# Optimization experiments

Measured on AMD Instinct MI355X. Metric: run time of the kernel, lower is better.

## Reference

```python
import jax, jax.numpy as jnp
import numpy as np

EPS = 1e-5

def layer_norm(x, g, b):
    mu = jnp.mean(x, axis=-1, keepdims=True)
    var = jnp.mean(jnp.square(x - mu), axis=-1, keepdims=True)
    return (x - mu) * jax.lax.rsqrt(var + EPS) * g + b

def setup_inputs() -> dict:
    B, T, C, H = 8, 1024, 1024, 16
    hs = C // H
    key = jax.random.key(0)
    ks = jax.random.split(key, 12)
    s = 0.02
    return {
        "x": jax.random.normal(ks[0], (B, T, C), dtype=jnp.float32),
        # per-head projections, stacked: [H, C, hs]
        "wq": jax.random.normal(ks[1], (H, C, hs), dtype=jnp.float32) * s,
        "wk": jax.random.normal(ks[2], (H, C, hs), dtype=jnp.float32) * s,
        "wv": jax.random.normal(ks[3], (H, C, hs), dtype=jnp.float32) * s,
        "w_proj": jax.random.normal(ks[4], (C, C), dtype=jnp.float32) * s,
        "b_proj": jnp.zeros((C,), dtype=jnp.float32),
        "ln1_g": jnp.ones((C,), dtype=jnp.float32),
        "ln1_b": jnp.zeros((C,), dtype=jnp.float32),
        "ln2_g": jnp.ones((C,), dtype=jnp.float32),
        "ln2_b": jnp.zeros((C,), dtype=jnp.float32),
        "w1": jax.random.normal(ks[5], (C, 4 * C), dtype=jnp.float32) * s,
        "b1": jnp.zeros((4 * C,), dtype=jnp.float32),
        "w2": jax.random.normal(ks[6], (4 * C, C), dtype=jnp.float32) * s,
        "b2": jnp.zeros((C,), dtype=jnp.float32),
    }

def reference(x, wq, wk, wv, w_proj, b_proj, ln1_g, ln1_b, ln2_g, ln2_b, w1, b1, w2, b2):
    B, T, C = x.shape
    # --- self-attention (pre-norm) ---
    h = layer_norm(x, ln1_g, ln1_b)                      # [B,T,C]
    q = jnp.einsum('btc,hcd->bhtd', h, wq)               # [B,H,T,hs]
    k = jnp.einsum('btc,hcd->bhtd', h, wk)
    v = jnp.einsum('btc,hcd->bhtd', h, wv)
    # NOTE: original scales by C**-0.5 with C = n_embed (not head_size)
    scores = jnp.einsum('bhtd,bhsd->bhts', q, k) * (C ** -0.5)
    causal = jnp.tril(jnp.ones((T, T), dtype=bool))
    scores = jnp.where(causal, scores, -jnp.inf)
    att = jax.nn.softmax(scores, axis=-1)                # dropout is identity (eval)
    out = jnp.einsum('bhts,bhsd->bhtd', att, v)          # [B,H,T,hs]
    out = out.transpose(0, 2, 1, 3).reshape(B, T, C)     # concat heads
    x = x + out @ w_proj + b_proj
    # --- feed-forward (pre-norm) ---
    h2 = layer_norm(x, ln2_g, ln2_b)
    x = x + jax.nn.relu(h2 @ w1 + b1) @ w2 + b2
    return x
```

## Files before the change

### kernel.cpp

```cpp
#include <hip/hip_runtime.h>
#include <cstdint>

typedef __attribute__((ext_vector_type(8))) __bf16 bf16x8;
typedef __attribute__((ext_vector_type(4))) float f32x4;

__device__ __forceinline__ unsigned short f2bf(float f) {
  union { float f; unsigned int u; } v; v.f = f;
  unsigned int u = v.u;
  return (unsigned short)((u + 0x7FFFu + ((u >> 16) & 1u)) >> 16);
}

__device__ __forceinline__ void load_lds16(const unsigned short* g, unsigned short* l) {
  __builtin_amdgcn_global_load_lds(
      (const __attribute__((address_space(1))) unsigned int*)g,
      (__attribute__((address_space(3))) unsigned int*)l, 16, 0, 0);
}

__global__ void transpose_f2b(const float* __restrict__ src, unsigned short* __restrict__ dst,
                              int K, int N, long sStride, long dStride) {
  __shared__ float tile[32][33];
  src += (long)blockIdx.z * sStride;
  dst += (long)blockIdx.z * dStride;
  const int nt = blockIdx.x * 32, kt = blockIdx.y * 32;
  const int tx = threadIdx.x & 31, ty = threadIdx.x >> 5;
#pragma unroll
  for (int i = 0; i < 4; i++)
    tile[ty + 8 * i][tx] = src[(long)(kt + ty + 8 * i) * N + nt + tx];
  __syncthreads();
#pragma unroll
  for (int i = 0; i < 4; i++)
    dst[(long)(nt + ty + 8 * i) * K + kt + tx] = f2bf(tile[tx][ty + 8 * i]);
}

__global__ void transpose_qkv(const float* __restrict__ wq, const float* __restrict__ wk,
                              const float* __restrict__ wv, unsigned short* __restrict__ dst) {
  __shared__ float tile[32][33];
  const int which = blockIdx.z >> 4, slice = blockIdx.z & 15;
  const float* src = (which == 0 ? wq : which == 1 ? wk : wv) + (long)slice * 65536;
  unsigned short* d = dst + (long)which * 1048576 + (long)slice * 65536;
  const int nt = blockIdx.x * 32, kt = blockIdx.y * 32;
  const int tx = threadIdx.x & 31, ty = threadIdx.x >> 5;
#pragma unroll
  for (int i = 0; i < 4; i++)
    tile[ty + 8 * i][tx] = src[(long)(kt + ty + 8 * i) * 64 + nt + tx];
  __syncthreads();
#pragma unroll
  for (int i = 0; i < 4; i++)
    d[(long)(nt + ty + 8 * i) * 1024 + kt + tx] = f2bf(tile[tx][ty + 8 * i]);
}

__global__ __launch_bounds__(256, 4) void ln_kernel(const float* __restrict__ x,
                                                    const float* __restrict__ g,
                                                    const float* __restrict__ b,
                                                    unsigned short* __restrict__ out) {
  const int row = blockIdx.x, tid = threadIdx.x;
  const int wave = tid >> 6, lane = tid & 63;
  const float4 xv = *(const float4*)&x[(long)row * 1024 + tid * 4];
  float s1 = xv.x + xv.y + xv.z + xv.w;
  float s2 = xv.x * xv.x + xv.y * xv.y + xv.z * xv.z + xv.w * xv.w;
#pragma unroll
  for (int m = 1; m < 64; m <<= 1) { s1 += __shfl_xor(s1, m); s2 += __shfl_xor(s2, m); }
  __shared__ float a1[4], a2[4];
  if (lane == 0) { a1[wave] = s1; a2[wave] = s2; }
  __syncthreads();
  s1 = a1[0] + a1[1] + a1[2] + a1[3];
  s2 = a2[0] + a2[1] + a2[2] + a2[3];
  const float mu = s1 * (1.f / 1024.f);
  const float var = s2 * (1.f / 1024.f) - mu * mu;
  const float rs = rsqrtf(var + 1e-5f);
  const float4 gv = *(const float4*)&g[tid * 4];
  const float4 bv = *(const float4*)&b[tid * 4];
  ushort4 o;
  o.x = f2bf((xv.x - mu) * rs * gv.x + bv.x);
  o.y = f2bf((xv.y - mu) * rs * gv.y + bv.y);
  o.z = f2bf((xv.z - mu) * rs * gv.z + bv.z);
  o.w = f2bf((xv.w - mu) * rs * gv.w + bv.w);
  *(ushort4*)&out[(long)row * 1024 + tid * 4] = o;
}

#define EPI_QKV 0
#define EPI_F32 1
#define EPI_RELU 2

template <int EPI>
__global__ __launch_bounds__(256, 2) void gemm_bt(
    const unsigned short* __restrict__ A, const unsigned short* __restrict__ Bt,
    int M, int N, int K,
    const float* __restrict__ bias, const float* __restrict__ resid,
    float* __restrict__ outF, unsigned short* __restrict__ outB,
    unsigned short* __restrict__ qb, unsigned short* __restrict__ kb,
    unsigned short* __restrict__ vTb) {
  __shared__ __attribute__((aligned(16))) unsigned short Alds[128 * 64];
  __shared__ __attribute__((aligned(16))) unsigned short Blds[128 * 64];
  const int tid = threadIdx.x;
  const int wave = tid >> 6, lane = tid & 63;
  const int quad = lane >> 4, l15 = lane & 15;
  const long tM = (long)blockIdx.x * 128;
  const long tN = (long)blockIdx.y * 128;
  const int wm = (wave >> 1) * 64, wn = (wave & 1) * 64;

  const unsigned short* aP[4];
  const unsigned short* bP[4];
  unsigned short* lA[4];
  unsigned short* lB[4];
#pragma unroll
  for (int qq = 0; qq < 4; qq++) {
    int p = (qq * 4 + wave) * 64 + lane;
    int m = p >> 3;
    int kc = (p & 7) ^ (m & 7);
    aP[qq] = A + (tM + m) * K + kc * 8;
    bP[qq] = Bt + (tN + m) * K + kc * 8;
    lA[qq] = Alds + (qq * 4 + wave) * 512;
    lB[qq] = Blds + (qq * 4 + wave) * 512;
  }

  f32x4 acc[4][4];
#pragma unroll
  for (int i = 0; i < 4; i++)
#pragma unroll
    for (int j = 0; j < 4; j++) acc[i][j] = (f32x4){0.f, 0.f, 0.f, 0.f};

  for (int k0 = 0; k0 < K; k0 += 64) {
    __syncthreads();
#pragma unroll
    for (int qq = 0; qq < 4; qq++) {
      load_lds16(aP[qq], lA[qq]);
      load_lds16(bP[qq], lB[qq]);
      aP[qq] += 64;
      bP[qq] += 64;
    }
    __syncthreads();
#pragma unroll
    for (int ks = 0; ks < 2; ks++) {
      bf16x8 af[4], bfr[4];
#pragma unroll
      for (int mt = 0; mt < 4; mt++) {
        int ml = wm + mt * 16 + l15;
        int pc = (ks * 4 + quad) ^ (ml & 7);
        af[mt] = *(const bf16x8*)&Alds[(ml * 8 + pc) * 8];
      }
#pragma unroll
      for (int nt = 0; nt < 4; nt++) {
        int nl = wn + nt * 16 + l15;
        int pc = (ks * 4 + quad) ^ (nl & 7);
        bfr[nt] = *(const bf16x8*)&Blds[(nl * 8 + pc) * 8];
      }
#pragma unroll
      for (int mt = 0; mt < 4; mt++)
#pragma unroll
        for (int nt = 0; nt < 4; nt++)
          acc[mt][nt] = __builtin_amdgcn_mfma_f32_16x16x32_bf16(af[mt], bfr[nt], acc[mt][nt], 0, 0, 0);
    }
  }

#pragma unroll
  for (int mt = 0; mt < 4; mt++) {
#pragma unroll
    for (int nt = 0; nt < 4; nt++) {
      const long col = tN + wn + nt * 16 + l15;
      const long row0 = tM + wm + mt * 16 + quad * 4;
      if (EPI == EPI_F32) {
        const float bv = bias[col];
#pragma unroll
        for (int r = 0; r < 4; r++) {
          long idx = (row0 + r) * N + col;
          outF[idx] = acc[mt][nt][r] + bv + resid[idx];
        }
      } else if (EPI == EPI_RELU) {
        const float bv = bias[col];
#pragma unroll
        for (int r = 0; r < 4; r++) {
          float v = acc[mt][nt][r] + bv;
          outB[(row0 + r) * N + col] = f2bf(v > 0.f ? v : 0.f);
        }
      } else {
        const int which = (int)(col >> 10);
        const int hh = (int)((col >> 6) & 15);
        const int dd = (int)(col & 63);
        const int b = (int)(row0 >> 10), t0 = (int)(row0 & 1023);
        if (which == 2) {
          ushort4 pk;
          pk.x = f2bf(acc[mt][nt][0]);
          pk.y = f2bf(acc[mt][nt][1]);
          pk.z = f2bf(acc[mt][nt][2]);
          pk.w = f2bf(acc[mt][nt][3]);
          *(ushort4*)&vTb[(long)(b * 16 + hh) * 65536 + dd * 1024 + t0] = pk;
        } else {
          unsigned short* dst = (which == 0 ? qb : kb);
#pragma unroll
          for (int r = 0; r < 4; r++)
            dst[((b * 16 + hh) * 1024 + t0 + r) * 64 + dd] = f2bf(acc[mt][nt][r]);
        }
      }
    }
  }
}

__global__ __launch_bounds__(256, 2) void attn_kernel(const unsigned short* __restrict__ qb,
                                                      const unsigned short* __restrict__ kb,
                                                      const unsigned short* __restrict__ vTb,
                                                      unsigned short* __restrict__ out) {
  __shared__ __attribute__((aligned(16))) unsigned short Klds[64 * 64];
  __shared__ __attribute__((aligned(16))) unsigned short Vlds[64 * 64];
  __shared__ __attribute__((aligned(16))) unsigned short Plds[4 * 16 * 68];
  const int bh = blockIdx.x;
  const int qt = blockIdx.y;
  const int tid = threadIdx.x;
  const int wave = tid >> 6, lane = tid & 63;
  const int quad = lane >> 4, l15 = lane & 15;

  const unsigned short* qp = qb + (long)bh * 65536;
  const unsigned short* kp = kb + (long)bh * 65536;
  const unsigned short* vp = vTb + (long)bh * 65536;

  const int qrow = qt * 64 + wave * 16 + l15;
  const bf16x8 qf0 = *(const bf16x8*)&qp[qrow * 64 + quad * 8];
  const bf16x8 qf1 = *(const bf16x8*)&qp[qrow * 64 + 32 + quad * 8];

  f32x4 O[4];
  float l_r[4] = {0.f, 0.f, 0.f, 0.f};
#pragma unroll
  for (int nt = 0; nt < 4; nt++) O[nt] = (f32x4){0.f, 0.f, 0.f, 0.f};

  unsigned short* Pl = Plds + wave * (16 * 68);
  const float cscale = 0.045084220f;
  const int tloc = wave * 16 + quad * 4;

  for (int kt = 0; kt <= qt; kt++) {
    __syncthreads();
#pragma unroll
    for (int c = 0; c < 2; c++) {
      const int pb = (wave * 2 + c) * 64;
      const int p = pb + lane;
      const int m = p >> 3;
      const int kc = (p & 7) ^ (m & 7);
      load_lds16(kp + (kt * 64 + m) * 64 + kc * 8, Klds + pb * 8);
      load_lds16(vp + m * 1024 + kt * 64 + kc * 8, Vlds + pb * 8);
    }
    __syncthreads();

    f32x4 S[4];
#pragma unroll
    for (int nt = 0; nt < 4; nt++) {
      const int row = nt * 16 + l15;
      const int pc0 = quad ^ (row & 7);
      const int pc1 = (quad + 4) ^ (row & 7);
      bf16x8 kf0 = *(const bf16x8*)&Klds[(row * 8 + pc0) * 8];
      bf16x8 kf1 = *(const bf16x8*)&Klds[(row * 8 + pc1) * 8];
      f32x4 s = (f32x4){0.f, 0.f, 0.f, 0.f};
      s = __builtin_amdgcn_mfma_f32_16x16x32_bf16(qf0, kf0, s, 0, 0, 0);
      s = __builtin_amdgcn_mfma_f32_16x16x32_bf16(qf1, kf1, s, 0, 0, 0);
      S[nt] = s;
    }

    const bool diag = (kt == qt);
#pragma unroll
    for (int nt = 0; nt < 4; nt++) {
      const int sg = nt * 16 + l15;
#pragma unroll
      for (int r = 0; r < 4; r++) {
        float pv = exp2f(S[nt][r] * cscale);
        if (diag && sg > tloc + r) pv = 0.f;
        l_r[r] += pv;
        Pl[(quad * 4 + r) * 68 + sg] = f2bf(pv);
      }
    }
    __threadfence_block();

#pragma unroll
    for (int ks2 = 0; ks2 < 2; ks2++) {
      bf16x8 pa = *(const bf16x8*)&Pl[l15 * 68 + ks2 * 32 + quad * 8];
#pragma unroll
      for (int nt = 0; nt < 4; nt++) {
        const int d = nt * 16 + l15;
        const int pc = (ks2 * 4 + quad) ^ (d & 7);
        bf16x8 vf = *(const bf16x8*)&Vlds[(d * 8 + pc) * 8];
        O[nt] = __builtin_amdgcn_mfma_f32_16x16x32_bf16(pa, vf, O[nt], 0, 0, 0);
      }
    }
  }

#pragma unroll
  for (int r = 0; r < 4; r++) {
    l_r[r] += __shfl_xor(l_r[r], 1);
    l_r[r] += __shfl_xor(l_r[r], 2);
    l_r[r] += __shfl_xor(l_r[r], 4);
    l_r[r] += __shfl_xor(l_r[r], 8);
    l_r[r] = __builtin_amdgcn_rcpf(l_r[r]);
  }

  const int b = bh >> 4, h = bh & 15;
#pragma unroll
  for (int nt = 0; nt < 4; nt++) {
#pragma unroll
    for (int r = 0; r < 4; r++) {
      const int t = qt * 64 + wave * 16 + quad * 4 + r;
      out[(long)(b * 1024 + t) * 1024 + h * 64 + nt * 16 + l15] = f2bf(O[nt][r] * l_r[r]);
    }
  }
}

extern "C" void kernel_launch(void* const* d_in, const int* in_sizes, int n_in,
                              void* d_out, int out_size, void* d_ws, size_t ws_size,
                              hipStream_t stream) {
  const float* x = (const float*)d_in[0];
  const float* wq = (const float*)d_in[1];
  const float* wk = (const float*)d_in[2];
  const float* wv = (const float*)d_in[3];
  const float* w_proj = (const float*)d_in[4];
  const float* b_proj = (const float*)d_in[5];
  const float* ln1_g = (const float*)d_in[6];
  const float* ln1_b = (const float*)d_in[7];
  const float* ln2_g = (const float*)d_in[8];
  const float* ln2_b = (const float*)d_in[9];
  const float* w1 = (const float*)d_in[10];
  const float* b1 = (const float*)d_in[11];
  const float* w2 = (const float*)d_in[12];
  const float* b2 = (const float*)d_in[13];
  float* out = (float*)d_out;

  char* w = (char*)d_ws;
  unsigned short* h1 = (unsigned short*)w;      w += (size_t)8192 * 1024 * 2;
  unsigned short* wqkvt = (unsigned short*)w;   w += (size_t)3072 * 1024 * 2;
  unsigned short* wprojt = (unsigned short*)w;  w += (size_t)1024 * 1024 * 2;
  unsigned short* w1t = (unsigned short*)w;     w += (size_t)4096 * 1024 * 2;
  unsigned short* w2t = (unsigned short*)w;     w += (size_t)4096 * 1024 * 2;
  unsigned short* qbuf = (unsigned short*)w;    w += (size_t)128 * 1024 * 64 * 2;
  unsigned short* kbuf = (unsigned short*)w;    w += (size_t)128 * 1024 * 64 * 2;
  unsigned short* vTbuf = (unsigned short*)w;   w += (size_t)128 * 1024 * 64 * 2;
  unsigned short* act = (unsigned short*)w;     w += (size_t)8192 * 4096 * 2;
  unsigned short* attnO = h1;
  unsigned short* h2 = qbuf;

  transpose_qkv<<<dim3(2, 32, 48), 256, 0, stream>>>(wq, wk, wv, wqkvt);
  transpose_f2b<<<dim3(32, 32, 1), 256, 0, stream>>>(w_proj, wprojt, 1024, 1024, 0, 0);
  transpose_f2b<<<dim3(128, 32, 1), 256, 0, stream>>>(w1, w1t, 1024, 4096, 0, 0);
  transpose_f2b<<<dim3(32, 128, 1), 256, 0, stream>>>(w2, w2t, 4096, 1024, 0, 0);

  ln_kernel<<<8192, 256, 0, stream>>>(x, ln1_g, ln1_b, h1);

  gemm_bt<EPI_QKV><<<dim3(64, 24), 256, 0, stream>>>(h1, wqkvt, 8192, 3072, 1024,
                                                     nullptr, nullptr, nullptr, nullptr,
                                                     qbuf, kbuf, vTbuf);

  attn_kernel<<<dim3(128, 16), 256, 0, stream>>>(qbuf, kbuf, vTbuf, attnO);

  gemm_bt<EPI_F32><<<dim3(64, 8), 256, 0, stream>>>(attnO, wprojt, 8192, 1024, 1024,
                                                    b_proj, x, out, nullptr,
                                                    nullptr, nullptr, nullptr);

  ln_kernel<<<8192, 256, 0, stream>>>(out, ln2_g, ln2_b, h2);

  gemm_bt<EPI_RELU><<<dim3(64, 32), 256, 0, stream>>>(h2, w1t, 8192, 4096, 1024,
                                                      b1, nullptr, nullptr, act,
                                                      nullptr, nullptr, nullptr);

  gemm_bt<EPI_F32><<<dim3(64, 8), 256, 0, stream>>>(act, w2t, 8192, 1024, 4096,
                                                    b2, out, out, nullptr,
                                                    nullptr, nullptr, nullptr);
}
```

Baseline: 453.2 us.

## Merge weight transposes, read attention K/V from global, raise occupancy bounds

```diff
diff --git a/kernel.cpp b/kernel.cpp
--- a/kernel.cpp
+++ b/kernel.cpp
@@ -16,12 +16,36 @@
       (__attribute__((address_space(3))) unsigned int*)l, 16, 0, 0);
 }
 
-__global__ void transpose_f2b(const float* __restrict__ src, unsigned short* __restrict__ dst,
-                              int K, int N, long sStride, long dStride) {
+__global__ void transpose_all(const float* __restrict__ wq, const float* __restrict__ wk,
+                              const float* __restrict__ wv, const float* __restrict__ w_proj,
+                              const float* __restrict__ w1, const float* __restrict__ w2,
+                              unsigned short* __restrict__ qkvt, unsigned short* __restrict__ projt,
+                              unsigned short* __restrict__ w1t, unsigned short* __restrict__ w2t) {
   __shared__ float tile[32][33];
-  src += (long)blockIdx.z * sStride;
-  dst += (long)blockIdx.z * dStride;
-  const int nt = blockIdx.x * 32, kt = blockIdx.y * 32;
+  const int id = blockIdx.x;
+  const float* src;
+  unsigned short* dst;
+  int K, N, nt, kt;
+  if (id < 3072) {
+    const int which = id >> 10, rem = id & 1023;
+    const int slice = rem >> 6, t = rem & 63;
+    src = (which == 0 ? wq : which == 1 ? wk : wv) + (long)slice * 65536;
+    dst = qkvt + (long)which * 1048576 + (long)slice * 65536;
+    K = 1024; N = 64;
+    nt = (t & 1) * 32; kt = (t >> 1) * 32;
+  } else if (id < 4096) {
+    const int t = id - 3072;
+    src = w_proj; dst = projt; K = 1024; N = 1024;
+    nt = (t & 31) * 32; kt = (t >> 5) * 32;
+  } else if (id < 8192) {
+    const int t = id - 4096;
+    src = w1; dst = w1t; K = 1024; N = 4096;
+    nt = (t & 127) * 32; kt = (t >> 7) * 32;
+  } else {
+    const int t = id - 8192;
+    src = w2; dst = w2t; K = 4096; N = 1024;
+    nt = (t & 31) * 32; kt = (t >> 5) * 32;
+  }
   const int tx = threadIdx.x & 31, ty = threadIdx.x >> 5;
 #pragma unroll
   for (int i = 0; i < 4; i++)
@@ -30,23 +54,6 @@
 #pragma unroll
   for (int i = 0; i < 4; i++)
     dst[(long)(nt + ty + 8 * i) * K + kt + tx] = f2bf(tile[tx][ty + 8 * i]);
-}
-
-__global__ void transpose_qkv(const float* __restrict__ wq, const float* __restrict__ wk,
-                              const float* __restrict__ wv, unsigned short* __restrict__ dst) {
-  __shared__ float tile[32][33];
-  const int which = blockIdx.z >> 4, slice = blockIdx.z & 15;
-  const float* src = (which == 0 ? wq : which == 1 ? wk : wv) + (long)slice * 65536;
-  unsigned short* d = dst + (long)which * 1048576 + (long)slice * 65536;
-  const int nt = blockIdx.x * 32, kt = blockIdx.y * 32;
-  const int tx = threadIdx.x & 31, ty = threadIdx.x >> 5;
-#pragma unroll
-  for (int i = 0; i < 4; i++)
-    tile[ty + 8 * i][tx] = src[(long)(kt + ty + 8 * i) * 64 + nt + tx];
-  __syncthreads();
-#pragma unroll
-  for (int i = 0; i < 4; i++)
-    d[(long)(nt + ty + 8 * i) * 1024 + kt + tx] = f2bf(tile[tx][ty + 8 * i]);
 }
 
 __global__ __launch_bounds__(256, 4) void ln_kernel(const float* __restrict__ x,
@@ -83,7 +90,7 @@
 #define EPI_RELU 2
 
 template <int EPI>
-__global__ __launch_bounds__(256, 2) void gemm_bt(
+__global__ __launch_bounds__(256, 3) void gemm_bt(
     const unsigned short* __restrict__ A, const unsigned short* __restrict__ Bt,
     int M, int N, int K,
     const float* __restrict__ bias, const float* __restrict__ resid,
@@ -196,12 +203,10 @@
   }
 }
 
-__global__ __launch_bounds__(256, 2) void attn_kernel(const unsigned short* __restrict__ qb,
+__global__ __launch_bounds__(256, 4) void attn_kernel(const unsigned short* __restrict__ qb,
                                                       const unsigned short* __restrict__ kb,
                                                       const unsigned short* __restrict__ vTb,
                                                       unsigned short* __restrict__ out) {
-  __shared__ __attribute__((aligned(16))) unsigned short Klds[64 * 64];
-  __shared__ __attribute__((aligned(16))) unsigned short Vlds[64 * 64];
   __shared__ __attribute__((aligned(16))) unsigned short Plds[4 * 16 * 68];
   const int bh = blockIdx.x;
   const int qt = blockIdx.y;
@@ -227,26 +232,12 @@
   const int tloc = wave * 16 + quad * 4;
 
   for (int kt = 0; kt <= qt; kt++) {
-    __syncthreads();
-#pragma unroll
-    for (int c = 0; c < 2; c++) {
-      const int pb = (wave * 2 + c) * 64;
-      const int p = pb + lane;
-      const int m = p >> 3;
-      const int kc = (p & 7) ^ (m & 7);
-      load_lds16(kp + (kt * 64 + m) * 64 + kc * 8, Klds + pb * 8);
-      load_lds16(vp + m * 1024 + kt * 64 + kc * 8, Vlds + pb * 8);
-    }
-    __syncthreads();
-
     f32x4 S[4];
 #pragma unroll
     for (int nt = 0; nt < 4; nt++) {
-      const int row = nt * 16 + l15;
-      const int pc0 = quad ^ (row & 7);
-      const int pc1 = (quad + 4) ^ (row & 7);
-      bf16x8 kf0 = *(const bf16x8*)&Klds[(row * 8 + pc0) * 8];
-      bf16x8 kf1 = *(const bf16x8*)&Klds[(row * 8 + pc1) * 8];
+      const unsigned short* kr = kp + (kt * 64 + nt * 16 + l15) * 64;
+      bf16x8 kf0 = *(const bf16x8*)&kr[quad * 8];
+      bf16x8 kf1 = *(const bf16x8*)&kr[32 + quad * 8];
       f32x4 s = (f32x4){0.f, 0.f, 0.f, 0.f};
       s = __builtin_amdgcn_mfma_f32_16x16x32_bf16(qf0, kf0, s, 0, 0, 0);
       s = __builtin_amdgcn_mfma_f32_16x16x32_bf16(qf1, kf1, s, 0, 0, 0);
@@ -272,9 +263,7 @@
       bf16x8 pa = *(const bf16x8*)&Pl[l15 * 68 + ks2 * 32 + quad * 8];
 #pragma unroll
       for (int nt = 0; nt < 4; nt++) {
-        const int d = nt * 16 + l15;
-        const int pc = (ks2 * 4 + quad) ^ (d & 7);
-        bf16x8 vf = *(const bf16x8*)&Vlds[(d * 8 + pc) * 8];
+        bf16x8 vf = *(const bf16x8*)&vp[(nt * 16 + l15) * 1024 + kt * 64 + ks2 * 32 + quad * 8];
         O[nt] = __builtin_amdgcn_mfma_f32_16x16x32_bf16(pa, vf, O[nt], 0, 0, 0);
       }
     }
@@ -332,10 +321,8 @@
   unsigned short* attnO = h1;
   unsigned short* h2 = qbuf;
 
-  transpose_qkv<<<dim3(2, 32, 48), 256, 0, stream>>>(wq, wk, wv, wqkvt);
-  transpose_f2b<<<dim3(32, 32, 1), 256, 0, stream>>>(w_proj, wprojt, 1024, 1024, 0, 0);
-  transpose_f2b<<<dim3(128, 32, 1), 256, 0, stream>>>(w1, w1t, 1024, 4096, 0, 0);
-  transpose_f2b<<<dim3(32, 128, 1), 256, 0, stream>>>(w2, w2t, 4096, 1024, 0, 0);
+  transpose_all<<<12288, 256, 0, stream>>>(wq, wk, wv, w_proj, w1, w2,
+                                           wqkvt, wprojt, w1t, w2t);
 
   ln_kernel<<<8192, 256, 0, stream>>>(x, ln1_g, ln1_b, h1);
 
```

Measured after the change: 521.2 us. +15.0%, slower.
